# Kernel tuning notes

Measured on AMD Instinct MI355X. Metric: run time of the kernel, lower is better.

The kernel has to match this reference:

```python
import jax, jax.numpy as jnp
import numpy as np

ENTRY_SIZE = 8192
TUPLE_SIZE = 16
N_NEURONS = ENTRY_SIZE // TUPLE_SIZE            # 512
ADDR_SPACE = 2 ** TUPLE_SIZE                     # 65536
BATCH = 4096


def setup_inputs() -> dict:
    key = jax.random.key(0)
    k1, k2, k3 = jax.random.split(key, 3)
    # Binary input bits [B, entry_size]
    inp = jax.random.randint(k1, (BATCH, ENTRY_SIZE), 0, 2, dtype=jnp.int32)
    # Permutation mapping bits -> tuples (identity permutation; arange fill)
    tuple_mapping = jnp.arange(ENTRY_SIZE, dtype=jnp.int64)
    # Dense RAM tables emulating the per-neuron dicts:
    #   counts[n, a] = number of training samples that hit address a in neuron n
    #                  (0 means the address was never trained -> not in dict)
    #   sums[n, a]   = accumulated target sum for that address
    counts = jax.random.randint(k2, (N_NEURONS, ADDR_SPACE), 0, 4, dtype=jnp.int32)
    sums = jax.random.normal(k3, (N_NEURONS, ADDR_SPACE), dtype=jnp.float32)
    return {"input": inp, "tuple_mapping": tuple_mapping, "counts": counts, "sums": sums}


def reference(input, tuple_mapping, counts, sums):
    """RegressionWisard.predict with centrality='mean'.

    input:  [B, entry_size] binary bits (int32)
    tuple_mapping: [entry_size] permutation (int)
    counts: [n_neurons, 2^tuple_size] int32 RAM hit counts
    sums:   [n_neurons, 2^tuple_size] float32 RAM target sums
    """
    B = input.shape[0]
    # Map and group bits into tuples: [B, N, T]
    mapped = jnp.take(input, tuple_mapping, axis=1).reshape(B, N_NEURONS, TUPLE_SIZE)
    # Binary address per (sample, neuron); tidx flips so bit 0 is the MSB.
    pow2 = (jnp.int32(1) << jnp.arange(TUPLE_SIZE - 1, -1, -1, dtype=jnp.int32))
    addr = jnp.einsum("bnt,t->bn", mapped, pow2)  # [B, N], values in [0, 2^T)
    neuron_idx = jnp.arange(N_NEURONS, dtype=jnp.int32)[None, :]  # [1, N]
    c = counts[neuron_idx, addr]  # [B, N]
    s = sums[neuron_idx, addr]    # [B, N]
    trained = c > 0               # dict-membership (torch.isin) equivalent
    response = jnp.sum(jnp.where(trained, s, jnp.float32(0)), axis=1)      # [B]
    counters = jnp.sum(jnp.where(trained, c, 0), axis=1).astype(s.dtype)   # [B]
    return jnp.nan_to_num(response / counters)
```

## Files before the change

### kernel.cpp

```cpp
#include <hip/hip_runtime.h>


constexpr int BATCH   = 4096;
constexpr int ENTRY   = 8192;
constexpr int TUP     = 16;
constexpr int NEUR    = ENTRY / TUP;
constexpr int LINES   = 4096;
constexpr int THREADS = 256;

typedef int v4i __attribute__((ext_vector_type(4)));
typedef unsigned int uint;

__device__ __forceinline__ int pack16(v4i b0, v4i b1, v4i b2, v4i b3) {
    return ((b0.x & 1) << 15) | ((b0.y & 1) << 14)
         | ((b0.z & 1) << 13) | ((b0.w & 1) << 12)
         | ((b1.x & 1) << 11) | ((b1.y & 1) << 10)
         | ((b1.z & 1) <<  9) | ((b1.w & 1) <<  8)
         | ((b2.x & 1) <<  7) | ((b2.y & 1) <<  6)
         | ((b2.z & 1) <<  5) | ((b2.w & 1) <<  4)
         | ((b3.x & 1) <<  3) | ((b3.y & 1) <<  2)
         | ((b3.z & 1) <<  1) |  (b3.w & 1);
}

__device__ __forceinline__ int sel4(v4i v, int e01) {
    const int ab = (e01 & 1) ? v.y : v.x;
    const int cd = (e01 & 1) ? v.w : v.z;
    return (e01 & 2) ? cd : ab;
}
__device__ __forceinline__ int sel16(v4i v0, v4i v1, v4i v2, v4i v3, int e) {
    const int e2 = e & 3;
    const int a = sel4(v0, e2), b = sel4(v1, e2);
    const int c = sel4(v2, e2), d = sel4(v3, e2);
    const int ab = (e & 4) ? b : a;
    const int cd = (e & 4) ? d : c;
    return (e & 8) ? cd : ab;
}

__global__ __launch_bounds__(THREADS, 4) void wisard_addr(
    const int* __restrict__ input,
    const int* __restrict__ mapping,
    unsigned short* __restrict__ addr_t)
{
    const int lane = threadIdx.x & 63;
    const int w    = threadIdx.x >> 6;
    const int s    = blockIdx.x * 4 + w;
    const int* row = input + (size_t)s * ENTRY;

    #pragma unroll
    for (int j = 0; j < 2; ++j) {
        const int nb = j * 256 + lane * 4;
        int  m0s[4];
        bool cg [4];
        #pragma unroll
        for (int q = 0; q < 4; ++q) {
            const int* map_n = mapping + (nb + q) * TUP;
            const int m0 = map_n[0];
            bool contig = ((m0 & 3) == 0);
            #pragma unroll
            for (int t = 1; t < TUP; ++t) contig &= (map_n[t] == m0 + t);
            m0s[q] = m0; cg[q] = contig;
        }

        v4i buf[16];
        #pragma unroll
        for (int q = 0; q < 4; ++q) {
            if (cg[q]) {
                const v4i* p = reinterpret_cast<const v4i*>(row + m0s[q]);
                buf[q * 4 + 0] = __builtin_nontemporal_load(p);
                buf[q * 4 + 1] = __builtin_nontemporal_load(p + 1);
                buf[q * 4 + 2] = __builtin_nontemporal_load(p + 2);
                buf[q * 4 + 3] = __builtin_nontemporal_load(p + 3);
            } else {
                const int* map_n = mapping + (nb + q) * TUP;
                #pragma unroll
                for (int i = 0; i < 4; ++i) {
                    v4i t;
                    t.x = row[map_n[i * 4 + 0]];
                    t.y = row[map_n[i * 4 + 1]];
                    t.z = row[map_n[i * 4 + 2]];
                    t.w = row[map_n[i * 4 + 3]];
                    buf[q * 4 + i] = t;
                }
            }
        }

        const uint a0 = (uint)pack16(buf[0],  buf[1],  buf[2],  buf[3]);
        const uint a1 = (uint)pack16(buf[4],  buf[5],  buf[6],  buf[7]);
        const uint a2 = (uint)pack16(buf[8],  buf[9],  buf[10], buf[11]);
        const uint a3 = (uint)pack16(buf[12], buf[13], buf[14], buf[15]);

        uint2 st;
        st.x = a0 | (a1 << 16);
        st.y = a2 | (a3 << 16);
        *reinterpret_cast<uint2*>(&addr_t[(size_t)s * NEUR + nb]) = st;
    }
}

__global__ __launch_bounds__(THREADS, 4) void wisard_stream(
    const unsigned short* __restrict__ addr_t,
    const int*   __restrict__ counts,
    const float* __restrict__ sums,
    float2*      __restrict__ contrib)
{
    __shared__ uint hist[LINES];
    __shared__ uint sorted[BATCH];
    __shared__ uint ttot[THREADS];
    __shared__ uint wsum[4];

    const int tid  = threadIdx.x;
    const int lane = tid & 63;
    const int w    = tid >> 6;
    const int n = (blockIdx.x & 7) * 64 + (blockIdx.x >> 3);

    uint a[16];
    #pragma unroll
    for (int j = 0; j < 16; ++j)
        a[j] = addr_t[(size_t)(j * THREADS + tid) * NEUR + n];

    #pragma unroll
    for (int j = 0; j < 16; ++j) hist[j * THREADS + tid] = 0u;
    __syncthreads();
    #pragma unroll
    for (int j = 0; j < 16; ++j) atomicAdd(&hist[a[j] >> 4], 1u);
    __syncthreads();

    uint loc[16];
    uint run = 0;
    #pragma unroll
    for (int j = 0; j < 16; ++j) { loc[j] = run; run += hist[tid * 16 + j]; }
    ttot[tid] = run;
    __syncthreads();
    uint v = ttot[tid];
    #pragma unroll
    for (int off = 1; off < 64; off <<= 1) {
        const uint u = __shfl_up(v, off, 64);
        if (lane >= off) v += u;
    }
    if (lane == 63) wsum[w] = v;
    __syncthreads();
    uint woff = 0;
    for (int i = 0; i < w; ++i) woff += wsum[i];
    const uint excl = woff + v - run;
    #pragma unroll
    for (int j = 0; j < 16; ++j) hist[tid * 16 + j] = excl + loc[j];
    __syncthreads();

    #pragma unroll
    for (int j = 0; j < 16; ++j) {
        const uint pos = atomicAdd(&hist[a[j] >> 4], 1u);
        sorted[pos] = (a[j] << 12) | (uint)(j * THREADS + tid);
    }
    __syncthreads();

    const int* ci = counts + ((size_t)n << 16);
    const int* si = reinterpret_cast<const int*>(sums) + ((size_t)n << 16);
    float2*    cb = contrib + (size_t)n * BATCH;

    auto LD = [&](int L, v4i* c, v4i* s4) {
        const v4i* cp = reinterpret_cast<const v4i*>(ci + ((size_t)L << 4));
        const v4i* sp = reinterpret_cast<const v4i*>(si + ((size_t)L << 4));
        c[0] = cp[0]; c[1] = cp[1]; c[2] = cp[2]; c[3] = cp[3];
        s4[0] = sp[0]; s4[1] = sp[1]; s4[2] = sp[2]; s4[3] = sp[3];
    };
    auto SERVE = [&](int L, const v4i* c, const v4i* s4) {
        const uint beg = (L == 0) ? 0u : hist[L - 1];
        const uint end = hist[L];
        for (uint k = beg; k < end; ++k) {
            const uint pk = sorted[k];
            const int e  = (int)((pk >> 12) & 15u);
            const int sm = (int)(pk & 4095u);
            const int cv = sel16(c[0], c[1], c[2], c[3], e);
            const int sb = sel16(s4[0], s4[1], s4[2], s4[3], e);
            const bool tr = cv > 0;
            float2 o;
            o.x = tr ? __int_as_float(sb) : 0.0f;
            o.y = __int_as_float(tr ? cv : 0);
            cb[sm] = o;
        }
    };

    v4i cA[4], sA[4], cB[4], sB[4];
    LD(tid, cA, sA);
    #pragma unroll
    for (int j = 0; j < 16; j += 2) {
        LD((j + 1) * THREADS + tid, cB, sB);
        SERVE(j * THREADS + tid, cA, sA);
        if (j + 2 < 16) LD((j + 2) * THREADS + tid, cA, sA);
        SERVE((j + 1) * THREADS + tid, cB, sB);
    }
}

__global__ __launch_bounds__(THREADS) void wisard_final(
    const float2* __restrict__ contrib,
    float*        __restrict__ out)
{
    __shared__ float sr [4][16];
    __shared__ int   scn[4][16];
    const int tid  = threadIdx.x;
    const int lane = tid & 63;
    const int w    = tid >> 6;
    const int sloc = tid & 15;
    const int g    = tid >> 4;
    const int s    = blockIdx.x * 16 + sloc;

    float r = 0.0f; int c = 0;
    #pragma unroll 8
    for (int i = 0; i < NEUR / 16; ++i) {
        const int n = g + i * 16;
        const float2 vv = contrib[(size_t)n * BATCH + s];
        r += vv.x;
        c += __float_as_int(vv.y);
    }
    r += __shfl_down(r, 32, 64); c += __shfl_down(c, 32, 64);
    r += __shfl_down(r, 16, 64); c += __shfl_down(c, 16, 64);
    if (lane < 16) { sr[w][lane] = r; scn[w][lane] = c; }
    __syncthreads();
    if (tid < 16) {
        r = sr[0][tid] + sr[1][tid] + sr[2][tid] + sr[3][tid];
        c = scn[0][tid] + scn[1][tid] + scn[2][tid] + scn[3][tid];
        out[blockIdx.x * 16 + tid] = (c > 0) ? (r / (float)c) : 0.0f;
    }
}

__global__ __launch_bounds__(THREADS) void wisard_fallback(
    const int*   __restrict__ input,
    const int*   __restrict__ mapping,
    const int*   __restrict__ counts,
    const float* __restrict__ sums,
    float*       __restrict__ out)
{
    __shared__ float s_resp[2][THREADS / 64];
    __shared__ int   s_cnt [2][THREADS / 64];

    const int tid  = threadIdx.x;
    const int lane = tid & 63;
    const int wv   = tid >> 6;
    const int b0   = blockIdx.x * 2;

    int   cv[2][2];
    float sv[2][2];

    #pragma unroll
    for (int k = 0; k < 2; ++k) {
        const int n = tid + k * THREADS;
        const int* map_n = mapping + n * TUP;
        const int m0 = map_n[0];
        bool contig = ((m0 & 3) == 0);
        #pragma unroll
        for (int t = 1; t < TUP; ++t) contig &= (map_n[t] == m0 + t);
        #pragma unroll
        for (int s = 0; s < 2; ++s) {
            const int* row = input + (size_t)(b0 + s) * ENTRY;
            int a;
            if (contig) {
                const v4i* p = reinterpret_cast<const v4i*>(row + m0);
                a = pack16(__builtin_nontemporal_load(p),
                           __builtin_nontemporal_load(p + 1),
                           __builtin_nontemporal_load(p + 2),
                           __builtin_nontemporal_load(p + 3));
            } else {
                a = 0;
                #pragma unroll
                for (int t = 0; t < TUP; ++t) a = (a << 1) | (row[map_n[t]] & 1);
            }
            const size_t idx = ((size_t)n << 16) | (unsigned)a;
            cv[s][k] = counts[idx];
            sv[s][k] = sums[idx];
        }
    }

    float resp[2]; int cnt[2];
    #pragma unroll
    for (int s = 0; s < 2; ++s) {
        resp[s] = 0.0f; cnt[s] = 0;
        #pragma unroll
        for (int k = 0; k < 2; ++k) {
            const bool t = cv[s][k] > 0;
            resp[s] += t ? sv[s][k] : 0.0f;
            cnt [s] += t ? cv[s][k] : 0;
        }
    }
    #pragma unroll
    for (int s = 0; s < 2; ++s) {
        float r = resp[s]; int c = cnt[s];
        #pragma unroll
        for (int off = 32; off > 0; off >>= 1) {
            r += __shfl_down(r, off, 64);
            c += __shfl_down(c, off, 64);
        }
        if (lane == 0) { s_resp[s][wv] = r; s_cnt[s][wv] = c; }
    }
    __syncthreads();
    if (tid < 2) {
        float r = 0.0f; int c = 0;
        #pragma unroll
        for (int w = 0; w < THREADS / 64; ++w) { r += s_resp[tid][w]; c += s_cnt[tid][w]; }
        out[b0 + tid] = (c > 0) ? (r / (float)c) : 0.0f;
    }
}

extern "C" void kernel_launch(void* const* d_in, const int* in_sizes, int n_in,
                              void* d_out, int out_size, void* d_ws, size_t ws_size,
                              hipStream_t stream) {
    (void)in_sizes; (void)n_in; (void)out_size;
    const int*   input   = (const int*)d_in[0];
    const int*   mapping = (const int*)d_in[1];
    const int*   counts  = (const int*)d_in[2];
    const float* sums    = (const float*)d_in[3];
    float*       out     = (float*)d_out;

    const size_t contrib_bytes = (size_t)NEUR * BATCH * sizeof(float2);
    const size_t addr_bytes    = (size_t)BATCH * NEUR * sizeof(unsigned short);

    if (ws_size < contrib_bytes + addr_bytes || d_ws == nullptr) {
        wisard_fallback<<<BATCH / 2, THREADS, 0, stream>>>(
            input, mapping, counts, sums, out);
        return;
    }

    float2*         contrib = (float2*)d_ws;
    unsigned short* addr_t  = (unsigned short*)((char*)d_ws + contrib_bytes);

    wisard_addr<<<BATCH / 4, THREADS, 0, stream>>>(input, mapping, addr_t);
    wisard_stream<<<NEUR, THREADS, 0, stream>>>(addr_t, counts, sums, contrib);
    wisard_final<<<BATCH / 16, THREADS, 0, stream>>>(contrib, out);
}
```

Before: 439.3 us.

## Stage per-neuron contributions in LDS and widen blocks to 512 threads

The stream kernel moves to 512-thread blocks, each thread covering 8 cache lines instead of 16, and writes per-sample contributions into a shared-memory buffer. That buffer is then copied to global memory as fully coalesced stores, replacing scattered float2 stores. The address kernel also now handles 8 neurons per thread with 128-bit stores, and sched barriers pin the load/serve double-buffer order. The extra 32KB of LDS per block raises LDS use to about 66KB, which may limit how many blocks fit on a CU.

Result: faster. 419.1 us (-4.6%).

```diff
diff --git a/kernel.cpp b/kernel.cpp
--- a/kernel.cpp
+++ b/kernel.cpp
@@ -6,6 +6,7 @@
 constexpr int TUP     = 16;
 constexpr int NEUR    = ENTRY / TUP;
 constexpr int LINES   = 4096;
+constexpr int TB      = 512;
 constexpr int THREADS = 256;
 
 typedef int v4i __attribute__((ext_vector_type(4)));
@@ -36,98 +37,98 @@
     return (e & 8) ? cd : ab;
 }
 
-__global__ __launch_bounds__(THREADS, 4) void wisard_addr(
+__global__ __launch_bounds__(TB, 2) void wisard_addr(
     const int* __restrict__ input,
     const int* __restrict__ mapping,
     unsigned short* __restrict__ addr_t)
 {
     const int lane = threadIdx.x & 63;
     const int w    = threadIdx.x >> 6;
-    const int s    = blockIdx.x * 4 + w;
+    const int s    = blockIdx.x * 8 + w;
     const int* row = input + (size_t)s * ENTRY;
-
-    #pragma unroll
-    for (int j = 0; j < 2; ++j) {
-        const int nb = j * 256 + lane * 4;
-        int  m0s[4];
-        bool cg [4];
-        #pragma unroll
-        for (int q = 0; q < 4; ++q) {
+    const int nb   = lane * 8;
+
+    int  m0s[8];
+    bool cg [8];
+    #pragma unroll
+    for (int q = 0; q < 8; ++q) {
+        const int* map_n = mapping + (nb + q) * TUP;
+        const int m0 = map_n[0];
+        bool contig = ((m0 & 3) == 0);
+        #pragma unroll
+        for (int t = 1; t < TUP; ++t) contig &= (map_n[t] == m0 + t);
+        m0s[q] = m0; cg[q] = contig;
+    }
+
+    v4i buf[32];
+    #pragma unroll
+    for (int q = 0; q < 8; ++q) {
+        if (cg[q]) {
+            const v4i* p = reinterpret_cast<const v4i*>(row + m0s[q]);
+            buf[q * 4 + 0] = __builtin_nontemporal_load(p);
+            buf[q * 4 + 1] = __builtin_nontemporal_load(p + 1);
+            buf[q * 4 + 2] = __builtin_nontemporal_load(p + 2);
+            buf[q * 4 + 3] = __builtin_nontemporal_load(p + 3);
+        } else {
             const int* map_n = mapping + (nb + q) * TUP;
-            const int m0 = map_n[0];
-            bool contig = ((m0 & 3) == 0);
             #pragma unroll
-            for (int t = 1; t < TUP; ++t) contig &= (map_n[t] == m0 + t);
-            m0s[q] = m0; cg[q] = contig;
-        }
-
-        v4i buf[16];
-        #pragma unroll
-        for (int q = 0; q < 4; ++q) {
-            if (cg[q]) {
-                const v4i* p = reinterpret_cast<const v4i*>(row + m0s[q]);
-                buf[q * 4 + 0] = __builtin_nontemporal_load(p);
-                buf[q * 4 + 1] = __builtin_nontemporal_load(p + 1);
-                buf[q * 4 + 2] = __builtin_nontemporal_load(p + 2);
-                buf[q * 4 + 3] = __builtin_nontemporal_load(p + 3);
-            } else {
-                const int* map_n = mapping + (nb + q) * TUP;
-                #pragma unroll
-                for (int i = 0; i < 4; ++i) {
-                    v4i t;
-                    t.x = row[map_n[i * 4 + 0]];
-                    t.y = row[map_n[i * 4 + 1]];
-                    t.z = row[map_n[i * 4 + 2]];
-                    t.w = row[map_n[i * 4 + 3]];
-                    buf[q * 4 + i] = t;
-                }
+            for (int i = 0; i < 4; ++i) {
+                v4i t;
+                t.x = row[map_n[i * 4 + 0]];
+                t.y = row[map_n[i * 4 + 1]];
+                t.z = row[map_n[i * 4 + 2]];
+                t.w = row[map_n[i * 4 + 3]];
+                buf[q * 4 + i] = t;
             }
         }
-
-        const uint a0 = (uint)pack16(buf[0],  buf[1],  buf[2],  buf[3]);
-        const uint a1 = (uint)pack16(buf[4],  buf[5],  buf[6],  buf[7]);
-        const uint a2 = (uint)pack16(buf[8],  buf[9],  buf[10], buf[11]);
-        const uint a3 = (uint)pack16(buf[12], buf[13], buf[14], buf[15]);
-
-        uint2 st;
-        st.x = a0 | (a1 << 16);
-        st.y = a2 | (a3 << 16);
-        *reinterpret_cast<uint2*>(&addr_t[(size_t)s * NEUR + nb]) = st;
-    }
-}
-
-__global__ __launch_bounds__(THREADS, 4) void wisard_stream(
+    }
+
+    uint a[8];
+    #pragma unroll
+    for (int q = 0; q < 8; ++q)
+        a[q] = (uint)pack16(buf[q * 4], buf[q * 4 + 1], buf[q * 4 + 2], buf[q * 4 + 3]);
+
+    uint4 st;
+    st.x = a[0] | (a[1] << 16);
+    st.y = a[2] | (a[3] << 16);
+    st.z = a[4] | (a[5] << 16);
+    st.w = a[6] | (a[7] << 16);
+    *reinterpret_cast<uint4*>(&addr_t[(size_t)s * NEUR + nb]) = st;
+}
+
+__global__ __launch_bounds__(TB, 4) void wisard_stream(
     const unsigned short* __restrict__ addr_t,
     const int*   __restrict__ counts,
     const float* __restrict__ sums,
     float2*      __restrict__ contrib)
 {
-    __shared__ uint hist[LINES];
-    __shared__ uint sorted[BATCH];
-    __shared__ uint ttot[THREADS];
-    __shared__ uint wsum[4];
+    __shared__ uint   hist[LINES];
+    __shared__ uint   sorted[BATCH];
+    __shared__ float2 acc[BATCH];
+    __shared__ uint   ttot[TB];
+    __shared__ uint   wsum[TB / 64];
 
     const int tid  = threadIdx.x;
     const int lane = tid & 63;
     const int w    = tid >> 6;
     const int n = (blockIdx.x & 7) * 64 + (blockIdx.x >> 3);
 
-    uint a[16];
-    #pragma unroll
-    for (int j = 0; j < 16; ++j)
-        a[j] = addr_t[(size_t)(j * THREADS + tid) * NEUR + n];
-
-    #pragma unroll
-    for (int j = 0; j < 16; ++j) hist[j * THREADS + tid] = 0u;
-    __syncthreads();
-    #pragma unroll
-    for (int j = 0; j < 16; ++j) atomicAdd(&hist[a[j] >> 4], 1u);
-    __syncthreads();
-
-    uint loc[16];
+    uint a[8];
+    #pragma unroll
+    for (int j = 0; j < 8; ++j)
+        a[j] = addr_t[(size_t)(j * TB + tid) * NEUR + n];
+
+    #pragma unroll
+    for (int j = 0; j < 8; ++j) hist[j * TB + tid] = 0u;
+    __syncthreads();
+    #pragma unroll
+    for (int j = 0; j < 8; ++j) atomicAdd(&hist[a[j] >> 4], 1u);
+    __syncthreads();
+
+    uint loc[8];
     uint run = 0;
     #pragma unroll
-    for (int j = 0; j < 16; ++j) { loc[j] = run; run += hist[tid * 16 + j]; }
+    for (int j = 0; j < 8; ++j) { loc[j] = run; run += hist[tid * 8 + j]; }
     ttot[tid] = run;
     __syncthreads();
     uint v = ttot[tid];
@@ -139,54 +140,74 @@
     if (lane == 63) wsum[w] = v;
     __syncthreads();
     uint woff = 0;
-    for (int i = 0; i < w; ++i) woff += wsum[i];
+    #pragma unroll
+    for (int i = 0; i < TB / 64; ++i) woff += (i < w) ? wsum[i] : 0u;
     const uint excl = woff + v - run;
     #pragma unroll
-    for (int j = 0; j < 16; ++j) hist[tid * 16 + j] = excl + loc[j];
-    __syncthreads();
-
-    #pragma unroll
-    for (int j = 0; j < 16; ++j) {
+    for (int j = 0; j < 8; ++j) hist[tid * 8 + j] = excl + loc[j];
+    __syncthreads();
+
+    #pragma unroll
+    for (int j = 0; j < 8; ++j) {
         const uint pos = atomicAdd(&hist[a[j] >> 4], 1u);
-        sorted[pos] = (a[j] << 12) | (uint)(j * THREADS + tid);
+        sorted[pos] = (a[j] << 12) | (uint)(j * TB + tid);
     }
     __syncthreads();
 
     const int* ci = counts + ((size_t)n << 16);
     const int* si = reinterpret_cast<const int*>(sums) + ((size_t)n << 16);
-    float2*    cb = contrib + (size_t)n * BATCH;
-
-    auto LD = [&](int L, v4i* c, v4i* s4) {
-        const v4i* cp = reinterpret_cast<const v4i*>(ci + ((size_t)L << 4));
-        const v4i* sp = reinterpret_cast<const v4i*>(si + ((size_t)L << 4));
-        c[0] = cp[0]; c[1] = cp[1]; c[2] = cp[2]; c[3] = cp[3];
-        s4[0] = sp[0]; s4[1] = sp[1]; s4[2] = sp[2]; s4[3] = sp[3];
-    };
-    auto SERVE = [&](int L, const v4i* c, const v4i* s4) {
-        const uint beg = (L == 0) ? 0u : hist[L - 1];
-        const uint end = hist[L];
-        for (uint k = beg; k < end; ++k) {
-            const uint pk = sorted[k];
-            const int e  = (int)((pk >> 12) & 15u);
-            const int sm = (int)(pk & 4095u);
-            const int cv = sel16(c[0], c[1], c[2], c[3], e);
-            const int sb = sel16(s4[0], s4[1], s4[2], s4[3], e);
-            const bool tr = cv > 0;
-            float2 o;
-            o.x = tr ? __int_as_float(sb) : 0.0f;
-            o.y = __int_as_float(tr ? cv : 0);
-            cb[sm] = o;
-        }
-    };
-
-    v4i cA[4], sA[4], cB[4], sB[4];
-    LD(tid, cA, sA);
-    #pragma unroll
-    for (int j = 0; j < 16; j += 2) {
-        LD((j + 1) * THREADS + tid, cB, sB);
-        SERVE(j * THREADS + tid, cA, sA);
-        if (j + 2 < 16) LD((j + 2) * THREADS + tid, cA, sA);
-        SERVE((j + 1) * THREADS + tid, cB, sB);
+
+#define LD(L, P) \
+    { const v4i* cp_ = reinterpret_cast<const v4i*>(ci + ((size_t)(L) << 4)); \
+      const v4i* sp_ = reinterpret_cast<const v4i*>(si + ((size_t)(L) << 4)); \
+      c##P##0 = cp_[0]; c##P##1 = cp_[1]; c##P##2 = cp_[2]; c##P##3 = cp_[3]; \
+      s##P##0 = sp_[0]; s##P##1 = sp_[1]; s##P##2 = sp_[2]; s##P##3 = sp_[3]; } \
+    __builtin_amdgcn_sched_barrier(0);
+
+#define SERVE(L, P) \
+    { const uint beg_ = ((L) == 0) ? 0u : hist[(L) - 1]; \
+      const uint end_ = hist[(L)]; \
+      for (uint k_ = beg_; k_ < end_; ++k_) { \
+        const uint pk_ = sorted[k_]; \
+        const int e_  = (int)((pk_ >> 12) & 15u); \
+        const int sm_ = (int)(pk_ & 4095u); \
+        const int cv_ = sel16(c##P##0, c##P##1, c##P##2, c##P##3, e_); \
+        const int sb_ = sel16(s##P##0, s##P##1, s##P##2, s##P##3, e_); \
+        const bool tr_ = cv_ > 0; \
+        float2 o_; \
+        o_.x = tr_ ? __int_as_float(sb_) : 0.0f; \
+        o_.y = __int_as_float(tr_ ? cv_ : 0); \
+        acc[sm_] = o_; } }
+
+    v4i cA0, cA1, cA2, cA3, sA0, sA1, sA2, sA3;
+    v4i cB0, cB1, cB2, cB3, sB0, sB1, sB2, sB3;
+
+    LD(tid, A)
+    LD(TB + tid, B)
+    SERVE(tid, A)
+    LD(2 * TB + tid, A)
+    SERVE(TB + tid, B)
+    LD(3 * TB + tid, B)
+    SERVE(2 * TB + tid, A)
+    LD(4 * TB + tid, A)
+    SERVE(3 * TB + tid, B)
+    LD(5 * TB + tid, B)
+    SERVE(4 * TB + tid, A)
+    LD(6 * TB + tid, A)
+    SERVE(5 * TB + tid, B)
+    LD(7 * TB + tid, B)
+    SERVE(6 * TB + tid, A)
+    SERVE(7 * TB + tid, B)
+#undef LD
+#undef SERVE
+
+    __syncthreads();
+
+    float2* cb = contrib + (size_t)n * BATCH;
+    #pragma unroll
+    for (int j = 0; j < 8; ++j) {
+        const int sm = j * TB + tid;
+        cb[sm] = acc[sm];
     }
 }
 
@@ -321,7 +342,7 @@
     float2*         contrib = (float2*)d_ws;
     unsigned short* addr_t  = (unsigned short*)((char*)d_ws + contrib_bytes);
 
-    wisard_addr<<<BATCH / 4, THREADS, 0, stream>>>(input, mapping, addr_t);
-    wisard_stream<<<NEUR, THREADS, 0, stream>>>(addr_t, counts, sums, contrib);
+    wisard_addr<<<BATCH / 8, TB, 0, stream>>>(input, mapping, addr_t);
+    wisard_stream<<<NEUR, TB, 0, stream>>>(addr_t, counts, sums, contrib);
     wisard_final<<<BATCH / 16, THREADS, 0, stream>>>(contrib, out);
 }
```

## Stage RAM lines into LDS asynchronously and scatter results through shared accumulator

Applied to the files above, without the earlier changes.

The stream kernel now double-buffers each wave's 64-byte counts and sums lines into LDS with global_load_lds, waiting on vmcnt, instead of holding them in vector registers and selecting with sel16. Per-neuron results are scattered into a shared float2 buffer and then written to global memory coalesced, replacing random global stores. The address kernel is remapped so that each thread handles four consecutive (sample, neuron) words, with vectorized mapping loads, and the nontemporal hints are dropped. The LDS use grows to about 100KB per block, which lowers occupancy, and the correctness of the hand-written waitcnt depends on the compiler's instruction ordering.

New measurement: 377.6 us. 14.1% less time.

```diff
diff --git a/kernel.cpp b/kernel.cpp
--- a/kernel.cpp
+++ b/kernel.cpp
@@ -22,90 +22,69 @@
          | ((b3.z & 1) <<  1) |  (b3.w & 1);
 }
 
-__device__ __forceinline__ int sel4(v4i v, int e01) {
-    const int ab = (e01 & 1) ? v.y : v.x;
-    const int cd = (e01 & 1) ? v.w : v.z;
-    return (e01 & 2) ? cd : ab;
-}
-__device__ __forceinline__ int sel16(v4i v0, v4i v1, v4i v2, v4i v3, int e) {
-    const int e2 = e & 3;
-    const int a = sel4(v0, e2), b = sel4(v1, e2);
-    const int c = sel4(v2, e2), d = sel4(v3, e2);
-    const int ab = (e & 4) ? b : a;
-    const int cd = (e & 4) ? d : c;
-    return (e & 8) ? cd : ab;
-}
-
-__global__ __launch_bounds__(THREADS, 4) void wisard_addr(
+__global__ __launch_bounds__(THREADS) void wisard_addr(
     const int* __restrict__ input,
     const int* __restrict__ mapping,
     unsigned short* __restrict__ addr_t)
 {
-    const int lane = threadIdx.x & 63;
-    const int w    = threadIdx.x >> 6;
-    const int s    = blockIdx.x * 4 + w;
-    const int* row = input + (size_t)s * ENTRY;
-
-    #pragma unroll
-    for (int j = 0; j < 2; ++j) {
-        const int nb = j * 256 + lane * 4;
-        int  m0s[4];
-        bool cg [4];
-        #pragma unroll
-        for (int q = 0; q < 4; ++q) {
-            const int* map_n = mapping + (nb + q) * TUP;
-            const int m0 = map_n[0];
-            bool contig = ((m0 & 3) == 0);
+    const int t0 = (blockIdx.x * THREADS + threadIdx.x) * 4;
+
+    v4i buf[16];
+    #pragma unroll
+    for (int q = 0; q < 4; ++q) {
+        const int wd = t0 + q;
+        const int s  = wd >> 9;
+        const int n  = wd & 511;
+        const v4i* mp = reinterpret_cast<const v4i*>(mapping + n * TUP);
+        const v4i m0v = mp[0], m1v = mp[1], m2v = mp[2], m3v = mp[3];
+        const int m0 = m0v.x;
+        const bool contig = ((m0 & 3) == 0)
+            && (m1v.x == m0 + 4) && (m2v.x == m0 + 8) && (m3v.x == m0 + 12)
+            && (m0v.y == m0 + 1) && (m0v.z == m0 + 2) && (m0v.w == m0 + 3)
+            && (m1v.y == m0 + 5) && (m1v.z == m0 + 6) && (m1v.w == m0 + 7)
+            && (m2v.y == m0 + 9) && (m2v.z == m0 + 10) && (m2v.w == m0 + 11)
+            && (m3v.y == m0 + 13) && (m3v.z == m0 + 14) && (m3v.w == m0 + 15);
+        const int* row = input + (size_t)s * ENTRY;
+        if (contig) {
+            const v4i* p = reinterpret_cast<const v4i*>(row + m0);
+            buf[q * 4 + 0] = p[0];
+            buf[q * 4 + 1] = p[1];
+            buf[q * 4 + 2] = p[2];
+            buf[q * 4 + 3] = p[3];
+        } else {
+            const int* map_n = mapping + n * TUP;
             #pragma unroll
-            for (int t = 1; t < TUP; ++t) contig &= (map_n[t] == m0 + t);
-            m0s[q] = m0; cg[q] = contig;
-        }
-
-        v4i buf[16];
-        #pragma unroll
-        for (int q = 0; q < 4; ++q) {
-            if (cg[q]) {
-                const v4i* p = reinterpret_cast<const v4i*>(row + m0s[q]);
-                buf[q * 4 + 0] = __builtin_nontemporal_load(p);
-                buf[q * 4 + 1] = __builtin_nontemporal_load(p + 1);
-                buf[q * 4 + 2] = __builtin_nontemporal_load(p + 2);
-                buf[q * 4 + 3] = __builtin_nontemporal_load(p + 3);
-            } else {
-                const int* map_n = mapping + (nb + q) * TUP;
-                #pragma unroll
-                for (int i = 0; i < 4; ++i) {
-                    v4i t;
-                    t.x = row[map_n[i * 4 + 0]];
-                    t.y = row[map_n[i * 4 + 1]];
-                    t.z = row[map_n[i * 4 + 2]];
-                    t.w = row[map_n[i * 4 + 3]];
-                    buf[q * 4 + i] = t;
-                }
+            for (int i = 0; i < 4; ++i) {
+                v4i t;
+                t.x = row[map_n[i * 4 + 0]];
+                t.y = row[map_n[i * 4 + 1]];
+                t.z = row[map_n[i * 4 + 2]];
+                t.w = row[map_n[i * 4 + 3]];
+                buf[q * 4 + i] = t;
             }
         }
-
-        const uint a0 = (uint)pack16(buf[0],  buf[1],  buf[2],  buf[3]);
-        const uint a1 = (uint)pack16(buf[4],  buf[5],  buf[6],  buf[7]);
-        const uint a2 = (uint)pack16(buf[8],  buf[9],  buf[10], buf[11]);
-        const uint a3 = (uint)pack16(buf[12], buf[13], buf[14], buf[15]);
-
-        uint2 st;
-        st.x = a0 | (a1 << 16);
-        st.y = a2 | (a3 << 16);
-        *reinterpret_cast<uint2*>(&addr_t[(size_t)s * NEUR + nb]) = st;
-    }
-}
-
-__global__ __launch_bounds__(THREADS, 4) void wisard_stream(
+    }
+
+    ushort4 st;
+    st.x = (unsigned short)pack16(buf[0],  buf[1],  buf[2],  buf[3]);
+    st.y = (unsigned short)pack16(buf[4],  buf[5],  buf[6],  buf[7]);
+    st.z = (unsigned short)pack16(buf[8],  buf[9],  buf[10], buf[11]);
+    st.w = (unsigned short)pack16(buf[12], buf[13], buf[14], buf[15]);
+    *reinterpret_cast<ushort4*>(&addr_t[t0]) = st;
+}
+
+__global__ __launch_bounds__(THREADS) void wisard_stream(
     const unsigned short* __restrict__ addr_t,
     const int*   __restrict__ counts,
     const float* __restrict__ sums,
     float2*      __restrict__ contrib)
 {
-    __shared__ uint hist[LINES];
-    __shared__ uint sorted[BATCH];
-    __shared__ uint ttot[THREADS];
-    __shared__ uint wsum[4];
+    __shared__ uint           hist[LINES];
+    __shared__ unsigned short sorted[BATCH];
+    __shared__ float2         acc[BATCH];
+    __shared__ uint           ttot[THREADS];
+    __shared__ uint           wsum[4];
+    __shared__ __align__(16) unsigned char stage[4][2][8192];
 
     const int tid  = threadIdx.x;
     const int lane = tid & 63;
@@ -139,7 +118,8 @@
     if (lane == 63) wsum[w] = v;
     __syncthreads();
     uint woff = 0;
-    for (int i = 0; i < w; ++i) woff += wsum[i];
+    #pragma unroll
+    for (int i = 0; i < 4; ++i) woff += (i < w) ? wsum[i] : 0u;
     const uint excl = woff + v - run;
     #pragma unroll
     for (int j = 0; j < 16; ++j) hist[tid * 16 + j] = excl + loc[j];
@@ -148,45 +128,64 @@
     #pragma unroll
     for (int j = 0; j < 16; ++j) {
         const uint pos = atomicAdd(&hist[a[j] >> 4], 1u);
-        sorted[pos] = (a[j] << 12) | (uint)(j * THREADS + tid);
-    }
-    __syncthreads();
-
-    const int* ci = counts + ((size_t)n << 16);
-    const int* si = reinterpret_cast<const int*>(sums) + ((size_t)n << 16);
-    float2*    cb = contrib + (size_t)n * BATCH;
-
-    auto LD = [&](int L, v4i* c, v4i* s4) {
-        const v4i* cp = reinterpret_cast<const v4i*>(ci + ((size_t)L << 4));
-        const v4i* sp = reinterpret_cast<const v4i*>(si + ((size_t)L << 4));
-        c[0] = cp[0]; c[1] = cp[1]; c[2] = cp[2]; c[3] = cp[3];
-        s4[0] = sp[0]; s4[1] = sp[1]; s4[2] = sp[2]; s4[3] = sp[3];
-    };
-    auto SERVE = [&](int L, const v4i* c, const v4i* s4) {
-        const uint beg = (L == 0) ? 0u : hist[L - 1];
-        const uint end = hist[L];
-        for (uint k = beg; k < end; ++k) {
-            const uint pk = sorted[k];
-            const int e  = (int)((pk >> 12) & 15u);
-            const int sm = (int)(pk & 4095u);
-            const int cv = sel16(c[0], c[1], c[2], c[3], e);
-            const int sb = sel16(s4[0], s4[1], s4[2], s4[3], e);
-            const bool tr = cv > 0;
-            float2 o;
-            o.x = tr ? __int_as_float(sb) : 0.0f;
-            o.y = __int_as_float(tr ? cv : 0);
-            cb[sm] = o;
-        }
-    };
-
-    v4i cA[4], sA[4], cB[4], sB[4];
-    LD(tid, cA, sA);
-    #pragma unroll
-    for (int j = 0; j < 16; j += 2) {
-        LD((j + 1) * THREADS + tid, cB, sB);
-        SERVE(j * THREADS + tid, cA, sA);
-        if (j + 2 < 16) LD((j + 2) * THREADS + tid, cA, sA);
-        SERVE((j + 1) * THREADS + tid, cB, sB);
+        sorted[pos] = (unsigned short)(((a[j] & 15u) << 12) | (uint)(j * THREADS + tid));
+    }
+    __syncthreads();
+
+    const char* cbase = reinterpret_cast<const char*>(counts + ((size_t)n << 16));
+    const char* sbase = reinterpret_cast<const char*>(
+                            reinterpret_cast<const int*>(sums) + ((size_t)n << 16));
+
+#define STAGE(J, B) { \
+    const uint base_ = (uint)(((J) * 256 + w * 64) * 64); \
+    _Pragma("unroll") \
+    for (int i_ = 0; i_ < 4; ++i_) { \
+        __builtin_amdgcn_global_load_lds( \
+            (const __attribute__((address_space(1))) uint*)(cbase + base_ + i_ * 1024 + lane * 16), \
+            (__attribute__((address_space(3))) uint*)&stage[w][(B)][i_ * 1024], 16, 0, 0); \
+        __builtin_amdgcn_global_load_lds( \
+            (const __attribute__((address_space(1))) uint*)(sbase + base_ + i_ * 1024 + lane * 16), \
+            (__attribute__((address_space(3))) uint*)&stage[w][(B)][4096 + i_ * 1024], 16, 0, 0); \
+    } }
+
+#define SERVE(J, B) { \
+    const int L_ = (J) * 256 + tid; \
+    const uint beg_ = (L_ == 0) ? 0u : hist[L_ - 1]; \
+    const uint end_ = hist[L_]; \
+    const unsigned char* cs_ = &stage[w][(B)][(uint)lane * 64]; \
+    const unsigned char* ss_ = &stage[w][(B)][4096 + (uint)lane * 64]; \
+    for (uint k_ = beg_; k_ < end_; ++k_) { \
+        const uint pk_ = sorted[k_]; \
+        const int e_  = (int)(pk_ >> 12); \
+        const int sm_ = (int)(pk_ & 4095u); \
+        const int   cv_ = *reinterpret_cast<const int*>(cs_ + e_ * 4); \
+        const float sv_ = *reinterpret_cast<const float*>(ss_ + e_ * 4); \
+        const bool tr_ = cv_ > 0; \
+        float2 o_; \
+        o_.x = tr_ ? sv_ : 0.0f; \
+        o_.y = __int_as_float(tr_ ? cv_ : 0); \
+        acc[sm_] = o_; \
+    } }
+
+    STAGE(0, 0)
+    #pragma unroll 1
+    for (int j = 0; j < 15; ++j) {
+        STAGE(j + 1, (j + 1) & 1)
+        asm volatile("s_waitcnt vmcnt(8)" ::: "memory");
+        SERVE(j, j & 1)
+    }
+    asm volatile("s_waitcnt vmcnt(0)" ::: "memory");
+    SERVE(15, 1)
+#undef STAGE
+#undef SERVE
+
+    __syncthreads();
+
+    float2* cb = contrib + (size_t)n * BATCH;
+    #pragma unroll
+    for (int j = 0; j < 16; ++j) {
+        const int sm = j * THREADS + tid;
+        cb[sm] = acc[sm];
     }
 }
 
@@ -254,10 +253,7 @@
             int a;
             if (contig) {
                 const v4i* p = reinterpret_cast<const v4i*>(row + m0);
-                a = pack16(__builtin_nontemporal_load(p),
-                           __builtin_nontemporal_load(p + 1),
-                           __builtin_nontemporal_load(p + 2),
-                           __builtin_nontemporal_load(p + 3));
+                a = pack16(p[0], p[1], p[2], p[3]);
             } else {
                 a = 0;
                 #pragma unroll
@@ -321,7 +317,8 @@
     float2*         contrib = (float2*)d_ws;
     unsigned short* addr_t  = (unsigned short*)((char*)d_ws + contrib_bytes);
 
-    wisard_addr<<<BATCH / 4, THREADS, 0, stream>>>(input, mapping, addr_t);
+    wisard_addr<<<(BATCH * NEUR) / (THREADS * 4), THREADS, 0, stream>>>(
+        input, mapping, addr_t);
     wisard_stream<<<NEUR, THREADS, 0, stream>>>(addr_t, counts, sums, contrib);
     wisard_final<<<BATCH / 16, THREADS, 0, stream>>>(contrib, out);
 }
```
